# Kernel optimization log

Hardware: AMD Instinct MI355X
Metric: run time of the kernel (lower is better)

## Reference

```python
import jax, jax.numpy as jnp
import numpy as np

B = 4
NB = 8192   # points per batch
MB = 2048   # query points per batch
C_IN = 64
RADII = (0.2, 0.4)
NSAMPLES = (16, 32)
EPS = 1e-5


def setup_inputs() -> dict:
    key = jax.random.key(0)
    ks = jax.random.split(key, 8)
    inp = {}
    inp["xyz"] = jax.random.uniform(ks[0], (B * NB, 3), jnp.float32)
    inp["features"] = jax.random.normal(ks[1], (B * NB, C_IN), jnp.float32)
    inp["new_xyz"] = jax.random.uniform(ks[2], (B * MB, 3), jnp.float32)
    inp["xyz_batch_cnt"] = jnp.full((B,), NB, jnp.int32)
    inp["new_xyz_batch_cnt"] = jnp.full((B,), MB, jnp.int32)
    cin = C_IN + 3  # use_xyz=True concatenates relative xyz
    for s in range(2):
        k0, k1 = jax.random.split(ks[3 + s])
        inp[f"w{s}0"] = jax.random.normal(k0, (128, cin), jnp.float32) * (2.0 / cin) ** 0.5
        inp[f"g{s}0"] = jnp.ones((128,), jnp.float32)
        inp[f"b{s}0"] = jnp.zeros((128,), jnp.float32)
        inp[f"w{s}1"] = jax.random.normal(k1, (128, 128), jnp.float32) * (2.0 / 128) ** 0.5
        inp[f"g{s}1"] = jnp.ones((128,), jnp.float32)
        inp[f"b{s}1"] = jnp.zeros((128,), jnp.float32)
    return inp


def _ball_query(new_b, xyz_b, radius, nsample):
    # new_b: (B, M, 3), xyz_b: (B, N, 3)
    n = xyz_b.shape[1]
    # squared distances via the quadratic expansion (avoids (B,M,N,3) temp)
    d2 = (jnp.sum(new_b * new_b, -1)[:, :, None]
          + jnp.sum(xyz_b * xyz_b, -1)[:, None, :]
          - 2.0 * jnp.einsum('bmc,bnc->bmn', new_b, xyz_b))
    in_ball = d2 < radius * radius
    # first-nsample-in-original-order semantics of the CUDA ball query
    order_key = jnp.where(in_ball, jnp.arange(n, dtype=jnp.int32)[None, None, :], n)
    idxs = jnp.sort(order_key, axis=-1)[..., :nsample]        # (B, M, nsample)
    valid = idxs < n
    first = idxs[..., :1]                                     # pad with first found idx
    idx = jnp.where(valid, idxs, first)
    empty = ~valid[..., 0]                                    # no neighbor in ball
    idx = jnp.where(empty[..., None], 0, idx)
    return idx, empty


def _bn_relu(x, g, b):
    # training-mode BatchNorm2d over (M, nsample) per channel, then ReLU
    mean = jnp.mean(x, axis=(0, 1))
    var = jnp.var(x, axis=(0, 1))
    return jax.nn.relu((x - mean) * jax.lax.rsqrt(var + EPS) * g + b)


def _scale(xyz_b, feat_b, new_b, radius, nsample, w0, g0, b0, w1, g1, b1):
    idx, empty = _ball_query(new_b, xyz_b, radius, nsample)
    gather = jax.vmap(lambda pts, i: pts[i])                  # per-batch gather
    gx = gather(xyz_b, idx) - new_b[:, :, None, :]            # (B, M, ns, 3)
    gf = gather(feat_b, idx)                                  # (B, M, ns, C)
    g = jnp.concatenate([gx, gf], axis=-1)                    # use_xyz=True
    g = jnp.where(empty[..., None, None], 0.0, g)             # zero empty balls
    g = g.reshape(-1, nsample, g.shape[-1])                   # (M_total, ns, 3+C)
    h = _bn_relu(jnp.einsum('mnc,oc->mno', g, w0), g0, b0)    # shared 1x1 conv
    h = _bn_relu(jnp.einsum('mnc,oc->mno', h, w1), g1, b1)
    return jnp.max(h, axis=1)                                 # max_pool over ns


def reference(xyz, features, new_xyz, xyz_batch_cnt, new_xyz_batch_cnt,
              w00, g00, b00, w01, g01, b01,
              w10, g10, b10, w11, g11, b11):
    b = xyz_batch_cnt.shape[0]
    xyz_b = xyz.reshape(b, -1, 3)
    feat_b = features.reshape(b, -1, features.shape[-1])
    new_b = new_xyz.reshape(b, -1, 3)
    f0 = _scale(xyz_b, feat_b, new_b, RADII[0], NSAMPLES[0], w00, g00, b00, w01, g01, b01)
    f1 = _scale(xyz_b, feat_b, new_b, RADII[1], NSAMPLES[1], w10, g10, b10, w11, g11, b11)
    return new_xyz, jnp.concatenate([f0, f1], axis=1)         # (M_total, 256)
```

## Files before the change

kernel.cpp:

```cpp
#include <hip/hip_runtime.h>
#include <stdio.h>

#define NBP   8192
#define MTOT  8192
#define CIN   64
#define CO    128

#define EPR(...) do { fprintf(stderr, __VA_ARGS__); fflush(stderr); } while (0)

typedef short short8 __attribute__((ext_vector_type(8)));
typedef float floatx4 __attribute__((ext_vector_type(4)));
typedef unsigned short ushort;
typedef ushort ushort4v __attribute__((ext_vector_type(4)));

__device__ __forceinline__ ushort f2b(float f)
{
    union { unsigned int i; float f; } x; x.f = f;
    return (ushort)((x.i + 0x7fffu + ((x.i >> 16) & 1u)) >> 16);
}
__device__ __forceinline__ float b2f(ushort u)
{
    union { unsigned int i; float f; } x; x.i = ((unsigned int)u) << 16;
    return x.f;
}
__device__ __forceinline__ void split_rne(float v, ushort& h, ushort& l)
{
    ushort hh = f2b(v);
    h = hh; l = f2b(v - b2f(hh));
}

__global__ void __launch_bounds__(256, 1) StackSAModuleMSG_85761906966880_kernel(
    const float* __restrict__ nxyz, float* __restrict__ out, float* __restrict__ stats,
    const float* __restrict__ feat, ushort* __restrict__ fh,
    const float* __restrict__ xyz, float4* __restrict__ xyz4, double* __restrict__ ppd,
    const float* __restrict__ w00, const float* __restrict__ w01,
    const float* __restrict__ w10, const float* __restrict__ w11,
    ushort* __restrict__ wh00, ushort* __restrict__ wl00,
    ushort* __restrict__ wh01, ushort* __restrict__ wl01,
    ushort* __restrict__ wh10, ushort* __restrict__ wl10,
    ushort* __restrict__ wh11, ushort* __restrict__ wl11)
{
    int i = blockIdx.x * 256 + threadIdx.x;
    if (i < 1024) stats[i] = 0.f;
    if (i < MTOT*3) out[i] = nxyz[i];
    if (i < 128*128) {
        split_rne(w01[i], wh01[i], wl01[i]);
        split_rne(w11[i], wh11[i], wl11[i]);
    }
    if (i < 128*96) {
        int o = i / 96, kd = i - o*96;
        int c = (kd < 64) ? (kd + 3) : ((kd < 67) ? (kd - 64) : -1);
        float a = (c >= 0) ? w00[o*67 + c] : 0.f;
        split_rne(a, wh00[i], wl00[i]);
        float b = (c >= 0) ? w10[o*67 + c] : 0.f;
        split_rne(b, wh10[i], wl10[i]);
    }
    if (i < 4*NBP) {
        float x = xyz[3*i+0], y = xyz[3*i+1], z = xyz[3*i+2];
        xyz4[i] = make_float4(x, y, z, 0.f);
        double px = (double)x, py = (double)y, pz = (double)z;
        ppd[i] = px*px + py*py + pz*pz;
    }
    {
        float4 v = *(const float4*)(feat + (size_t)4*i);
        ushort4v h;
        h[0] = f2b(v.x); h[1] = f2b(v.y); h[2] = f2b(v.z); h[3] = f2b(v.w);
        *(ushort4v*)(fh + (size_t)4*i) = h;
    }
}

__global__ void __launch_bounds__(256, 1) sa_ballq(
    const float4* __restrict__ xyz4, const double* __restrict__ ppd,
    const float* __restrict__ new_xyz,
    int* __restrict__ idx0, int* __restrict__ idx1,
    int* __restrict__ empty0, int* __restrict__ empty1)
{
    const double r2a = 0.2 * 0.2;
    const double r2b = 0.4 * 0.4;
    int m    = blockIdx.x * 4 + (threadIdx.x >> 6);
    int lane = threadIdx.x & 63;
    int b    = m >> 11;
    int base = b * NBP;

    double nx = (double)new_xyz[3*m+0];
    double ny = (double)new_xyz[3*m+1];
    double nz = (double)new_xyz[3*m+2];
    double nn = nx*nx + ny*ny + nz*nz;

    int cnt0 = 0, cnt1 = 0;
    int first0 = base, first1 = base;
    unsigned long long lt = (1ull << lane) - 1ull;

    for (int j = 0; j < NBP; j += 64) {
        int gi = base + j + lane;
        float4 p = xyz4[gi];
        double px = (double)p.x;
        double py = (double)p.y;
        double pz = (double)p.z;
        double pp = ppd[gi];
        double dt = nx*px + ny*py + nz*pz;
        double d2 = nn + pp - 2.0*dt;
        bool in0 = d2 < r2a;
        bool in1 = d2 < r2b;
        unsigned long long m0 = __ballot(in0);
        unsigned long long m1 = __ballot(in1);
        if (in0) {
            int p0 = cnt0 + __popcll(m0 & lt);
            if (p0 < 16) idx0[m*16 + p0] = gi;
        }
        if (in1) {
            int p1 = cnt1 + __popcll(m1 & lt);
            if (p1 < 32) idx1[m*32 + p1] = gi;
        }
        if (cnt0 == 0 && m0) first0 = base + j + (__ffsll((long long)m0) - 1);
        if (cnt1 == 0 && m1) first1 = base + j + (__ffsll((long long)m1) - 1);
        cnt0 += __popcll(m0);
        cnt1 += __popcll(m1);
        if (cnt0 >= 16 && cnt1 >= 32) break;
    }
    int c0 = cnt0 < 16 ? cnt0 : 16;
    int c1 = cnt1 < 32 ? cnt1 : 32;
    if (lane >= c0 && lane < 16) idx0[m*16 + lane] = first0;
    if (lane >= c1 && lane < 32) idx1[m*32 + lane] = first1;
    if (lane == 0) { empty0[m] = (cnt0 == 0); empty1[m] = (cnt1 == 0); }
}

template<int NS, int GM>
__device__ __forceinline__ void stats1_body(
    const ushort* __restrict__ fh,
    const float* __restrict__ xyz, const float* __restrict__ nxyz,
    const int* __restrict__ idx, const int* __restrict__ empty,
    const ushort* __restrict__ wh0, float* __restrict__ part,
    int bx, int t, ushort* ah)
{
    int m0 = bx * GM;
    int wv = t >> 6, lane = t & 63, l16 = lane & 15, qo = lane >> 4;
    int n0 = 32*wv;

    short8 bh[3][2];
#pragma unroll
    for (int ks = 0; ks < 3; ks++)
#pragma unroll
        for (int nt = 0; nt < 2; nt++)
            bh[ks][nt] = *(const short8*)(wh0 +
                (long long)(n0 + 16*nt + l16)*96 + ks*32 + qo*8);

    unsigned em = 0;
#pragma unroll
    for (int g = 0; g < GM; g++) em |= (empty[m0 + g] ? 1u : 0u) << g;
    const long long ib = (long long)m0 * NS;
    int n1 = t >> 3, c8 = t & 7, n2 = n1 + 32;
    int n3 = t >> 2, k3 = t & 3;
    int gi1 = idx[ib + n1];
    int gi2 = idx[ib + n2];
    short8 vh1 = *(const short8*)(fh + (size_t)gi1*CIN + 8*c8);
    short8 vh2 = *(const short8*)(fh + (size_t)gi2*CIN + 8*c8);
    const short8 Z8 = {0,0,0,0,0,0,0,0};
    short8 vh3 = Z8;
    int g3 = n3 / NS;
    if (k3 == 0 && !((em >> g3) & 1u)) {
        int gi3 = idx[ib + n3];
#pragma unroll
        for (int c = 0; c < 3; c++)
            vh3[c] = (short)f2b(xyz[3*gi3+c] - nxyz[3*(m0+g3)+c]);
    }

    if ((em >> (n1 / NS)) & 1u) vh1 = Z8;
    if ((em >> (n2 / NS)) & 1u) vh2 = Z8;
    *(short8*)(ah + n1*136 + 8*c8) = vh1;
    *(short8*)(ah + n2*136 + 8*c8) = vh2;
    *(short8*)(ah + n3*136 + 64 + 8*k3) = vh3;
    __syncthreads();

    floatx4 acc[4][2];
#pragma unroll
    for (int i = 0; i < 4; i++) {
        acc[i][0] = (floatx4){0.f,0.f,0.f,0.f};
        acc[i][1] = (floatx4){0.f,0.f,0.f,0.f};
    }
#pragma unroll
    for (int ks = 0; ks < 3; ks++) {
        int kb = ks*32 + qo*8;
#pragma unroll
        for (int mt = 0; mt < 4; mt++) {
            int ao = (16*mt + l16)*136 + kb;
            short8 fh8 = *(const short8*)(ah + ao);
#pragma unroll
            for (int nt = 0; nt < 2; nt++)
                acc[mt][nt] = __builtin_amdgcn_mfma_f32_16x16x32_bf16(
                                  fh8, bh[ks][nt], acc[mt][nt], 0, 0, 0);
        }
    }

    float sum[2] = {0.f,0.f}, sq[2] = {0.f,0.f};
#pragma unroll
    for (int mt = 0; mt < 4; mt++)
#pragma unroll
        for (int nt = 0; nt < 2; nt++)
#pragma unroll
            for (int r = 0; r < 4; r++) {
                float a = acc[mt][nt][r];
                sum[nt] += a; sq[nt] = fmaf(a, a, sq[nt]);
            }
#pragma unroll
    for (int nt = 0; nt < 2; nt++) {
        sum[nt] += __shfl_xor(sum[nt], 16); sum[nt] += __shfl_xor(sum[nt], 32);
        sq[nt]  += __shfl_xor(sq[nt],  16); sq[nt]  += __shfl_xor(sq[nt],  32);
    }
    if (lane < 16) {
#pragma unroll
        for (int nt = 0; nt < 2; nt++) {
            int c = n0 + 16*nt + lane;
            part[(long long)bx*256 + c]       = sum[nt];
            part[(long long)bx*256 + 128 + c] = sq[nt];
        }
    }
}

__global__ void __launch_bounds__(256, 4) sa_stats1_both(
    const ushort* __restrict__ fh,
    const float* __restrict__ xyz, const float* __restrict__ nxyz,
    const int* __restrict__ idx0, const int* __restrict__ empty0,
    const ushort* __restrict__ wh00, float* __restrict__ partA,
    const int* __restrict__ idx1, const int* __restrict__ empty1,
    const ushort* __restrict__ wh10, float* __restrict__ partB)
{
    __shared__ ushort ah[64*136];
    int t = threadIdx.x;
    if (blockIdx.x < MTOT/4)
        stats1_body<16,4>(fh, xyz, nxyz, idx0, empty0, wh00, partA,
                          blockIdx.x, t, ah);
    else
        stats1_body<32,2>(fh, xyz, nxyz, idx1, empty1, wh10, partB,
                          blockIdx.x - MTOT/4, t, ah);
}

template<int NS, int GM>
__device__ __forceinline__ void fused_body(
    const ushort* __restrict__ fh,
    const float* __restrict__ xyz, const float* __restrict__ nxyz,
    const int* __restrict__ idx, const int* __restrict__ empty,
    const ushort* __restrict__ wh0, const ushort* __restrict__ wl0,
    const ushort* __restrict__ wh1, const ushort* __restrict__ wl1,
    const float* __restrict__ g0, const float* __restrict__ b0,
    const float* __restrict__ s1sum, const float* __restrict__ s1sq,
    float* __restrict__ part, float* __restrict__ mxo, float* __restrict__ mno,
    float invN, int bx, int t,
    ushort* ah, float* kv, float* sv)
{
    const int TPG = NS/16;
    int m0 = bx * GM;
    int wv = t >> 6, lane = t & 63, l16 = lane & 15, qo = lane >> 4;
    int n0 = 32*wv;

    if (t < 128) {
        float mean = s1sum[t] * invN;
        float var  = s1sq[t] * invN - mean * mean;
        float k    = rsqrtf(var + 1e-5f) * g0[t];
        kv[t] = k;
        sv[t] = b0[t] - mean * k;
    }

    short8 b1h[3][2], b1l[3][2];
#pragma unroll
    for (int ks = 0; ks < 3; ks++)
#pragma unroll
        for (int nt = 0; nt < 2; nt++) {
            long long wo = (long long)(n0 + 16*nt + l16)*96 + ks*32 + qo*8;
            b1h[ks][nt] = *(const short8*)(wh0 + wo);
            b1l[ks][nt] = *(const short8*)(wl0 + wo);
        }

    unsigned em = 0;
#pragma unroll
    for (int g = 0; g < GM; g++) em |= (empty[m0 + g] ? 1u : 0u) << g;
    const long long ib = (long long)m0 * NS;
    int n1 = t >> 3, c8 = t & 7, n2 = n1 + 32;
    int n3 = t >> 2, k3 = t & 3;
    int gi1 = idx[ib + n1];
    int gi2 = idx[ib + n2];
    short8 vh1 = *(const short8*)(fh + (size_t)gi1*CIN + 8*c8);
    short8 vh2 = *(const short8*)(fh + (size_t)gi2*CIN + 8*c8);
    const short8 Z8 = {0,0,0,0,0,0,0,0};
    short8 vh3 = Z8;
    int g3 = n3 / NS;
    if (k3 == 0 && !((em >> g3) & 1u)) {
        int gi3 = idx[ib + n3];
#pragma unroll
        for (int c = 0; c < 3; c++)
            vh3[c] = (short)f2b(xyz[3*gi3+c] - nxyz[3*(m0+g3)+c]);
    }

    if ((em >> (n1 / NS)) & 1u) vh1 = Z8;
    if ((em >> (n2 / NS)) & 1u) vh2 = Z8;
    *(short8*)(ah + n1*136 + 8*c8) = vh1;
    *(short8*)(ah + n2*136 + 8*c8) = vh2;
    *(short8*)(ah + n3*136 + 64 + 8*k3) = vh3;
    __syncthreads();

    {
        floatx4 acc[4][2];
#pragma unroll
        for (int i = 0; i < 4; i++) {
            acc[i][0] = (floatx4){0.f,0.f,0.f,0.f};
            acc[i][1] = (floatx4){0.f,0.f,0.f,0.f};
        }
#pragma unroll
        for (int ks = 0; ks < 3; ks++) {
            int kb = ks*32 + qo*8;
#pragma unroll
            for (int mt = 0; mt < 4; mt++) {
                int ao = (16*mt + l16)*136 + kb;
                short8 fh8 = *(const short8*)(ah + ao);
#pragma unroll
                for (int nt = 0; nt < 2; nt++) {
                    acc[mt][nt] = __builtin_amdgcn_mfma_f32_16x16x32_bf16(
                                      fh8, b1l[ks][nt], acc[mt][nt], 0, 0, 0);
                    acc[mt][nt] = __builtin_amdgcn_mfma_f32_16x16x32_bf16(
                                      fh8, b1h[ks][nt], acc[mt][nt], 0, 0, 0);
                }
            }
        }

        __syncthreads();
#pragma unroll
        for (int nt = 0; nt < 2; nt++) {
            int c = n0 + 16*nt + l16;
            float k = kv[c], s = sv[c];
#pragma unroll
            for (int mt = 0; mt < 4; mt++) {
#pragma unroll
                for (int r = 0; r < 4; r++) {
                    float h = fmaxf(fmaf(acc[mt][nt][r], k, s), 0.f);
                    int row = 16*mt + qo*4 + r;
                    ah[row*136 + c] = f2b(h);
                }
            }
        }

        short8 b2h[4][2], b2l[4][2];
#pragma unroll
        for (int ks = 0; ks < 4; ks++)
#pragma unroll
            for (int nt = 0; nt < 2; nt++) {
                long long wo = (long long)(n0 + 16*nt + l16)*128 + ks*32 + qo*8;
                b2h[ks][nt] = *(const short8*)(wh1 + wo);
                b2l[ks][nt] = *(const short8*)(wl1 + wo);
            }
        __syncthreads();

        floatx4 acc2[4][2];
#pragma unroll
        for (int i = 0; i < 4; i++) {
            acc2[i][0] = (floatx4){0.f,0.f,0.f,0.f};
            acc2[i][1] = (floatx4){0.f,0.f,0.f,0.f};
        }
#pragma unroll
        for (int ks = 0; ks < 4; ks++) {
            int kb = ks*32 + qo*8;
#pragma unroll
            for (int mt = 0; mt < 4; mt++) {
                int ao = (16*mt + l16)*136 + kb;
                short8 fh8 = *(const short8*)(ah + ao);
#pragma unroll
                for (int nt = 0; nt < 2; nt++) {
                    acc2[mt][nt] = __builtin_amdgcn_mfma_f32_16x16x32_bf16(
                                      fh8, b2l[ks][nt], acc2[mt][nt], 0, 0, 0);
                    acc2[mt][nt] = __builtin_amdgcn_mfma_f32_16x16x32_bf16(
                                      fh8, b2h[ks][nt], acc2[mt][nt], 0, 0, 0);
                }
            }
        }

        float sum[2] = {0.f,0.f}, sq[2] = {0.f,0.f};
        float Mx[GM][2], Mn[GM][2];
#pragma unroll
        for (int g = 0; g < GM; g++) {
            Mx[g][0] = -3.4e38f; Mx[g][1] = -3.4e38f;
            Mn[g][0] =  3.4e38f; Mn[g][1] =  3.4e38f;
        }
#pragma unroll
        for (int mt = 0; mt < 4; mt++) {
            int gg = mt / TPG;
#pragma unroll
            for (int nt = 0; nt < 2; nt++)
#pragma unroll
                for (int r = 0; r < 4; r++) {
                    float a = acc2[mt][nt][r];
                    sum[nt] += a; sq[nt] = fmaf(a, a, sq[nt]);
                    Mx[gg][nt] = fmaxf(Mx[gg][nt], a);
                    Mn[gg][nt] = fminf(Mn[gg][nt], a);
                }
        }
#pragma unroll
        for (int nt = 0; nt < 2; nt++) {
            sum[nt] += __shfl_xor(sum[nt], 16); sum[nt] += __shfl_xor(sum[nt], 32);
            sq[nt]  += __shfl_xor(sq[nt],  16); sq[nt]  += __shfl_xor(sq[nt],  32);
#pragma unroll
            for (int g = 0; g < GM; g++) {
                Mx[g][nt] = fmaxf(Mx[g][nt], __shfl_xor(Mx[g][nt], 16));
                Mx[g][nt] = fmaxf(Mx[g][nt], __shfl_xor(Mx[g][nt], 32));
                Mn[g][nt] = fminf(Mn[g][nt], __shfl_xor(Mn[g][nt], 16));
                Mn[g][nt] = fminf(Mn[g][nt], __shfl_xor(Mn[g][nt], 32));
            }
        }
        if (lane < 16) {
#pragma unroll
            for (int nt = 0; nt < 2; nt++) {
                int c = n0 + 16*nt + lane;
                part[(long long)bx*256 + c]       = sum[nt];
                part[(long long)bx*256 + 128 + c] = sq[nt];
#pragma unroll
                for (int g = 0; g < GM; g++) {
                    mxo[(long long)(m0+g)*128 + c] = Mx[g][nt];
                    mno[(long long)(m0+g)*128 + c] = Mn[g][nt];
                }
            }
        }
    }
}

__global__ void __launch_bounds__(256, 4) sa_fused_both(
    const ushort* __restrict__ fh,
    const float* __restrict__ xyz, const float* __restrict__ nxyz,
    const int* __restrict__ idx0, const int* __restrict__ empty0,
    const ushort* __restrict__ wh00, const ushort* __restrict__ wl00,
    const ushort* __restrict__ wh01, const ushort* __restrict__ wl01,
    const float* __restrict__ g00, const float* __restrict__ b00,
    const float* __restrict__ s1sumA, const float* __restrict__ s1sqA,
    float* __restrict__ partA, float* __restrict__ mx0, float* __restrict__ mn0,
    float invN0,
    const int* __restrict__ idx1, const int* __restrict__ empty1,
    const ushort* __restrict__ wh10, const ushort* __restrict__ wl10,
    const ushort* __restrict__ wh11, const ushort* __restrict__ wl11,
    const float* __restrict__ g10, const float* __restrict__ b10,
    const float* __restrict__ s1sumB, const float* __restrict__ s1sqB,
    float* __restrict__ partB, float* __restrict__ mx1, float* __restrict__ mn1,
    float invN1)
{
    __shared__ ushort ah[64*136];
    __shared__ float kv[128], sv[128];
    int t = threadIdx.x;
    if (blockIdx.x < MTOT/4)
        fused_body<16,4>(fh, xyz, nxyz, idx0, empty0,
                         wh00, wl00, wh01, wl01, g00, b00, s1sumA, s1sqA,
                         partA, mx0, mn0, invN0, blockIdx.x, t,
                         ah, kv, sv);
    else
        fused_body<32,2>(fh, xyz, nxyz, idx1, empty1,
                         wh10, wl10, wh11, wl11, g10, b10, s1sumB, s1sqB,
                         partB, mx1, mn1, invN1, blockIdx.x - MTOT/4, t,
                         ah, kv, sv);
}

__global__ void __launch_bounds__(256, 1) sa_reduce2(
    const float* __restrict__ partA, int nbA, float* __restrict__ dstA,
    const float* __restrict__ partB, int nbB, float* __restrict__ dstB)
{
    __shared__ float red[256];
    int t = threadIdx.x;
    const float* part; float* dst; int nb, b;
    if (blockIdx.x < 256) { part = partA; dst = dstA; nb = nbA; b = blockIdx.x; }
    else                  { part = partB; dst = dstB; nb = nbB; b = blockIdx.x - 256; }
    float s = 0.f;
    for (int i = t; i < nb; i += 256) s += part[(long long)i*256 + b];
    red[t] = s;
    __syncthreads();
    for (int off = 128; off > 0; off >>= 1) {
        if (t < off) red[t] += red[t + off];
        __syncthreads();
    }
    if (t == 0) dst[b] = red[0];
}

__global__ void __launch_bounds__(256, 1) sa_pass3b(
    const float* __restrict__ mx0, const float* __restrict__ mn0,
    const float* __restrict__ g01, const float* __restrict__ b01,
    const float* __restrict__ mx1, const float* __restrict__ mn1,
    const float* __restrict__ g11, const float* __restrict__ b11,
    const float* __restrict__ stats, float* __restrict__ outp,
    float invN0, float invN1)
{
    int i = blockIdx.x * 256 + threadIdx.x;
    int m = i >> 8, o = i & 255;
    bool sc1 = o >= 128;
    int oc = o & 127;
    const float* sm = sc1 ? (stats + 768) : (stats + 256);
    const float* sp = sc1 ? (stats + 896) : (stats + 384);
    float invN = sc1 ? invN1 : invN0;
    float gg   = sc1 ? g11[oc] : g01[oc];
    float bb   = sc1 ? b11[oc] : b01[oc];
    float mean = sm[oc] * invN;
    float var  = sp[oc] * invN - mean * mean;
    float k    = rsqrtf(var + 1e-5f) * gg;
    float sh   = bb - mean * k;
    long long mi = (long long)m * 128 + oc;
    float v;
    if (k >= 0.f) v = sc1 ? mx1[mi] : mx0[mi];
    else          v = sc1 ? mn1[mi] : mn0[mi];
    float r = fmaf(v, k, sh);
    outp[i] = r > 0.f ? r : 0.f;
}

extern "C" void kernel_launch(void* const* d_in, const int* in_sizes, int n_in,
                              void* d_out, int out_size, void* d_ws, size_t ws_size,
                              hipStream_t stream)
{
    const float* xyz  = (const float*)d_in[0];
    const float* feat = (const float*)d_in[1];
    const float* nxyz = (const float*)d_in[2];
    const float* w00 = (const float*)d_in[5];
    const float* g00 = (const float*)d_in[6];
    const float* b00 = (const float*)d_in[7];
    const float* w01 = (const float*)d_in[8];
    const float* g01 = (const float*)d_in[9];
    const float* b01 = (const float*)d_in[10];
    const float* w10 = (const float*)d_in[11];
    const float* g10 = (const float*)d_in[12];
    const float* b10 = (const float*)d_in[13];
    const float* w11 = (const float*)d_in[14];
    const float* g11 = (const float*)d_in[15];
    const float* b11 = (const float*)d_in[16];
    float* out = (float*)d_out;

    char*  wsb    = (char*)d_ws;
    float* stats  = (float*)(wsb);
    int*   idx0   = (int*)(wsb + 4096);
    int*   idx1   = (int*)(wsb + 4096 + 524288);
    int*   empty0 = (int*)(wsb + 4096 + 524288 + 1048576);
    int*   empty1 = (int*)(wsb + 4096 + 524288 + 1048576 + 32768);
    ushort* fh    = (ushort*)(wsb + 2000000);
    float4* xyz4  = (float4*)(wsb + 13000000);
    double* ppd   = (double*)(wsb + 14000000);
    float* mx0    = (float*)(wsb + 150000000);
    float* mn0    = (float*)(wsb + 155000000);
    float* mx1    = (float*)(wsb + 160000000);
    float* mn1    = (float*)(wsb + 165000000);
    ushort* wh01  = (ushort*)(wsb + 170000000);
    ushort* wl01  = (ushort*)(wsb + 171000000);
    ushort* wh11  = (ushort*)(wsb + 172000000);
    ushort* wl11  = (ushort*)(wsb + 173000000);
    ushort* wh00  = (ushort*)(wsb + 174000000);
    ushort* wl00  = (ushort*)(wsb + 175000000);
    ushort* wh10  = (ushort*)(wsb + 176000000);
    ushort* wl10  = (ushort*)(wsb + 177000000);
    float* partA  = (float*)(wsb + 180000000);
    float* partB  = (float*)(wsb + 183000000);

    const float invN0 = 1.0f / (float)(MTOT*16);
    const float invN1 = 1.0f / (float)(MTOT*32);
    float* fout = out + MTOT*3;

    StackSAModuleMSG_85761906966880_kernel<<<2048, 256, 0, stream>>>(
        nxyz, out, stats, feat, fh, xyz, xyz4, ppd,
        w00, w01, w10, w11,
        wh00, wl00, wh01, wl01, wh10, wl10, wh11, wl11);

    sa_ballq<<<MTOT/4, 256, 0, stream>>>(xyz4, ppd, nxyz, idx0, idx1, empty0, empty1);

    sa_stats1_both<<<MTOT/4 + MTOT/2, 256, 0, stream>>>(
        fh, xyz, nxyz,
        idx0, empty0, wh00, partA,
        idx1, empty1, wh10, partB);

    sa_reduce2<<<512, 256, 0, stream>>>(partA, MTOT/4, stats + 0,
                                        partB, MTOT/2, stats + 512);

    sa_fused_both<<<MTOT/4 + MTOT/2, 256, 0, stream>>>(
        fh, xyz, nxyz,
        idx0, empty0, wh00, wl00, wh01, wl01, g00, b00,
        stats + 0, stats + 128, partA, mx0, mn0, invN0,
        idx1, empty1, wh10, wl10, wh11, wl11, g10, b10,
        stats + 512, stats + 640, partB, mx1, mn1, invN1);

    sa_reduce2<<<512, 256, 0, stream>>>(partA, MTOT/4, stats + 256,
                                        partB, MTOT/2, stats + 768);

    sa_pass3b<<<(MTOT*256)/256, 256, 0, stream>>>(
        mx0, mn0, g01, b01, mx1, mn1, g11, b11, stats, fout, invN0, invN1);

    hipError_t e = hipGetLastError();
    if (e != hipSuccess) EPR("[KL] enqueue err=%d (%s)\n", (int)e, hipGetErrorString(e));
}
```

Baseline: 239.7 us.

## Fuse ball query into prep kernel and replace partial-sum reductions with atomics

The ball-query kernel is merged into the preprocessing kernel as extra blocks. It now reads raw xyz and computes squared norms inline, so the float4/double staging buffers are no longer needed. The per-block partial BN statistics and the two separate reduce kernels are replaced by atomicAdd into the stats array, removing three launches and their global round trips. The A tile's LDS stride shrinks and a separate LDS buffer holds the hidden activations, which removes one __syncthreads. Weight register loads are also moved later, after the gathers. The cost is float atomic contention on 512 addresses and a summation order that is no longer deterministic.

```diff
diff --git a/kernel.cpp b/kernel.cpp
--- a/kernel.cpp
+++ b/kernel.cpp
@@ -5,6 +5,8 @@
 #define MTOT  8192
 #define CIN   64
 #define CO    128
+#define ASTR  104
+#define HSTR  136
 
 #define EPR(...) do { fprintf(stderr, __VA_ARGS__); fflush(stderr); } while (0)
 
@@ -30,9 +32,11 @@
 }
 
 __global__ void __launch_bounds__(256, 1) StackSAModuleMSG_85761906966880_kernel(
-    const float* __restrict__ nxyz, float* __restrict__ out, float* __restrict__ stats,
+    const float* __restrict__ xyz, const float* __restrict__ nxyz,
+    float* __restrict__ out, float* __restrict__ stats,
     const float* __restrict__ feat, ushort* __restrict__ fh,
-    const float* __restrict__ xyz, float4* __restrict__ xyz4, double* __restrict__ ppd,
+    int* __restrict__ idx0, int* __restrict__ idx1,
+    int* __restrict__ empty0, int* __restrict__ empty1,
     const float* __restrict__ w00, const float* __restrict__ w01,
     const float* __restrict__ w10, const float* __restrict__ w11,
     ushort* __restrict__ wh00, ushort* __restrict__ wl00,
@@ -40,89 +44,77 @@
     ushort* __restrict__ wh10, ushort* __restrict__ wl10,
     ushort* __restrict__ wh11, ushort* __restrict__ wl11)
 {
-    int i = blockIdx.x * 256 + threadIdx.x;
-    if (i < 1024) stats[i] = 0.f;
-    if (i < MTOT*3) out[i] = nxyz[i];
-    if (i < 128*128) {
-        split_rne(w01[i], wh01[i], wl01[i]);
-        split_rne(w11[i], wh11[i], wl11[i]);
-    }
-    if (i < 128*96) {
-        int o = i / 96, kd = i - o*96;
-        int c = (kd < 64) ? (kd + 3) : ((kd < 67) ? (kd - 64) : -1);
-        float a = (c >= 0) ? w00[o*67 + c] : 0.f;
-        split_rne(a, wh00[i], wl00[i]);
-        float b = (c >= 0) ? w10[o*67 + c] : 0.f;
-        split_rne(b, wh10[i], wl10[i]);
-    }
-    if (i < 4*NBP) {
-        float x = xyz[3*i+0], y = xyz[3*i+1], z = xyz[3*i+2];
-        xyz4[i] = make_float4(x, y, z, 0.f);
-        double px = (double)x, py = (double)y, pz = (double)z;
-        ppd[i] = px*px + py*py + pz*pz;
-    }
-    {
-        float4 v = *(const float4*)(feat + (size_t)4*i);
-        ushort4v h;
-        h[0] = f2b(v.x); h[1] = f2b(v.y); h[2] = f2b(v.z); h[3] = f2b(v.w);
-        *(ushort4v*)(fh + (size_t)4*i) = h;
-    }
-}
-
-__global__ void __launch_bounds__(256, 1) sa_ballq(
-    const float4* __restrict__ xyz4, const double* __restrict__ ppd,
-    const float* __restrict__ new_xyz,
-    int* __restrict__ idx0, int* __restrict__ idx1,
-    int* __restrict__ empty0, int* __restrict__ empty1)
-{
-    const double r2a = 0.2 * 0.2;
-    const double r2b = 0.4 * 0.4;
-    int m    = blockIdx.x * 4 + (threadIdx.x >> 6);
-    int lane = threadIdx.x & 63;
-    int b    = m >> 11;
-    int base = b * NBP;
-
-    double nx = (double)new_xyz[3*m+0];
-    double ny = (double)new_xyz[3*m+1];
-    double nz = (double)new_xyz[3*m+2];
-    double nn = nx*nx + ny*ny + nz*nz;
-
-    int cnt0 = 0, cnt1 = 0;
-    int first0 = base, first1 = base;
-    unsigned long long lt = (1ull << lane) - 1ull;
-
-    for (int j = 0; j < NBP; j += 64) {
-        int gi = base + j + lane;
-        float4 p = xyz4[gi];
-        double px = (double)p.x;
-        double py = (double)p.y;
-        double pz = (double)p.z;
-        double pp = ppd[gi];
-        double dt = nx*px + ny*py + nz*pz;
-        double d2 = nn + pp - 2.0*dt;
-        bool in0 = d2 < r2a;
-        bool in1 = d2 < r2b;
-        unsigned long long m0 = __ballot(in0);
-        unsigned long long m1 = __ballot(in1);
-        if (in0) {
-            int p0 = cnt0 + __popcll(m0 & lt);
-            if (p0 < 16) idx0[m*16 + p0] = gi;
-        }
-        if (in1) {
-            int p1 = cnt1 + __popcll(m1 & lt);
-            if (p1 < 32) idx1[m*32 + p1] = gi;
-        }
-        if (cnt0 == 0 && m0) first0 = base + j + (__ffsll((long long)m0) - 1);
-        if (cnt1 == 0 && m1) first1 = base + j + (__ffsll((long long)m1) - 1);
-        cnt0 += __popcll(m0);
-        cnt1 += __popcll(m1);
-        if (cnt0 >= 16 && cnt1 >= 32) break;
-    }
-    int c0 = cnt0 < 16 ? cnt0 : 16;
-    int c1 = cnt1 < 32 ? cnt1 : 32;
-    if (lane >= c0 && lane < 16) idx0[m*16 + lane] = first0;
-    if (lane >= c1 && lane < 32) idx1[m*32 + lane] = first1;
-    if (lane == 0) { empty0[m] = (cnt0 == 0); empty1[m] = (cnt1 == 0); }
+    if (blockIdx.x < MTOT/4) {
+        const double r2a = 0.2 * 0.2;
+        const double r2b = 0.4 * 0.4;
+        int m    = blockIdx.x * 4 + (threadIdx.x >> 6);
+        int lane = threadIdx.x & 63;
+        int b    = m >> 11;
+        int base = b * NBP;
+
+        double nx = (double)nxyz[3*m+0];
+        double ny = (double)nxyz[3*m+1];
+        double nz = (double)nxyz[3*m+2];
+        double nn = nx*nx + ny*ny + nz*nz;
+
+        int cnt0 = 0, cnt1 = 0;
+        int first0 = base, first1 = base;
+        unsigned long long lt = (1ull << lane) - 1ull;
+
+        for (int j = 0; j < NBP; j += 64) {
+            int gi = base + j + lane;
+            double px = (double)xyz[3*gi+0];
+            double py = (double)xyz[3*gi+1];
+            double pz = (double)xyz[3*gi+2];
+            double pp = px*px + py*py + pz*pz;
+            double dt = nx*px + ny*py + nz*pz;
+            double d2 = nn + pp - 2.0*dt;
+            bool in0 = d2 < r2a;
+            bool in1 = d2 < r2b;
+            unsigned long long m0 = __ballot(in0);
+            unsigned long long m1 = __ballot(in1);
+            if (in0) {
+                int p0 = cnt0 + __popcll(m0 & lt);
+                if (p0 < 16) idx0[m*16 + p0] = gi;
+            }
+            if (in1) {
+                int p1 = cnt1 + __popcll(m1 & lt);
+                if (p1 < 32) idx1[m*32 + p1] = gi;
+            }
+            if (cnt0 == 0 && m0) first0 = base + j + (__ffsll((long long)m0) - 1);
+            if (cnt1 == 0 && m1) first1 = base + j + (__ffsll((long long)m1) - 1);
+            cnt0 += __popcll(m0);
+            cnt1 += __popcll(m1);
+            if (cnt0 >= 16 && cnt1 >= 32) break;
+        }
+        int c0 = cnt0 < 16 ? cnt0 : 16;
+        int c1 = cnt1 < 32 ? cnt1 : 32;
+        if (lane >= c0 && lane < 16) idx0[m*16 + lane] = first0;
+        if (lane >= c1 && lane < 32) idx1[m*32 + lane] = first1;
+        if (lane == 0) { empty0[m] = (cnt0 == 0); empty1[m] = (cnt1 == 0); }
+    } else {
+        int i = (blockIdx.x - MTOT/4) * 256 + threadIdx.x;
+        if (i < 1024) stats[i] = 0.f;
+        if (i < MTOT*3) out[i] = nxyz[i];
+        if (i < 128*128) {
+            split_rne(w01[i], wh01[i], wl01[i]);
+            split_rne(w11[i], wh11[i], wl11[i]);
+        }
+        if (i < 128*96) {
+            int o = i / 96, kd = i - o*96;
+            int c = (kd < 64) ? (kd + 3) : ((kd < 67) ? (kd - 64) : -1);
+            float a = (c >= 0) ? w00[o*67 + c] : 0.f;
+            split_rne(a, wh00[i], wl00[i]);
+            float b = (c >= 0) ? w10[o*67 + c] : 0.f;
+            split_rne(b, wh10[i], wl10[i]);
+        }
+        {
+            float4 v = *(const float4*)(feat + (size_t)4*i);
+            ushort4v h;
+            h[0] = f2b(v.x); h[1] = f2b(v.y); h[2] = f2b(v.z); h[3] = f2b(v.w);
+            *(ushort4v*)(fh + (size_t)4*i) = h;
+        }
+    }
 }
 
 template<int NS, int GM>
@@ -130,20 +122,13 @@
     const ushort* __restrict__ fh,
     const float* __restrict__ xyz, const float* __restrict__ nxyz,
     const int* __restrict__ idx, const int* __restrict__ empty,
-    const ushort* __restrict__ wh0, float* __restrict__ part,
+    const ushort* __restrict__ wh0,
+    float* __restrict__ ssum, float* __restrict__ ssq,
     int bx, int t, ushort* ah)
 {
     int m0 = bx * GM;
     int wv = t >> 6, lane = t & 63, l16 = lane & 15, qo = lane >> 4;
     int n0 = 32*wv;
-
-    short8 bh[3][2];
-#pragma unroll
-    for (int ks = 0; ks < 3; ks++)
-#pragma unroll
-        for (int nt = 0; nt < 2; nt++)
-            bh[ks][nt] = *(const short8*)(wh0 +
-                (long long)(n0 + 16*nt + l16)*96 + ks*32 + qo*8);
 
     unsigned em = 0;
 #pragma unroll
@@ -165,11 +150,19 @@
             vh3[c] = (short)f2b(xyz[3*gi3+c] - nxyz[3*(m0+g3)+c]);
     }
 
+    short8 bh[3][2];
+#pragma unroll
+    for (int ks = 0; ks < 3; ks++)
+#pragma unroll
+        for (int nt = 0; nt < 2; nt++)
+            bh[ks][nt] = *(const short8*)(wh0 +
+                (long long)(n0 + 16*nt + l16)*96 + ks*32 + qo*8);
+
     if ((em >> (n1 / NS)) & 1u) vh1 = Z8;
     if ((em >> (n2 / NS)) & 1u) vh2 = Z8;
-    *(short8*)(ah + n1*136 + 8*c8) = vh1;
-    *(short8*)(ah + n2*136 + 8*c8) = vh2;
-    *(short8*)(ah + n3*136 + 64 + 8*k3) = vh3;
+    *(short8*)(ah + n1*ASTR + 8*c8) = vh1;
+    *(short8*)(ah + n2*ASTR + 8*c8) = vh2;
+    *(short8*)(ah + n3*ASTR + 64 + 8*k3) = vh3;
     __syncthreads();
 
     floatx4 acc[4][2];
@@ -183,7 +176,7 @@
         int kb = ks*32 + qo*8;
 #pragma unroll
         for (int mt = 0; mt < 4; mt++) {
-            int ao = (16*mt + l16)*136 + kb;
+            int ao = (16*mt + l16)*ASTR + kb;
             short8 fh8 = *(const short8*)(ah + ao);
 #pragma unroll
             for (int nt = 0; nt < 2; nt++)
@@ -211,8 +204,8 @@
 #pragma unroll
         for (int nt = 0; nt < 2; nt++) {
             int c = n0 + 16*nt + lane;
-            part[(long long)bx*256 + c]       = sum[nt];
-            part[(long long)bx*256 + 128 + c] = sq[nt];
+            atomicAdd(&ssum[c], sum[nt]);
+            atomicAdd(&ssq[c],  sq[nt]);
         }
     }
 }
@@ -221,18 +214,18 @@
     const ushort* __restrict__ fh,
     const float* __restrict__ xyz, const float* __restrict__ nxyz,
     const int* __restrict__ idx0, const int* __restrict__ empty0,
-    const ushort* __restrict__ wh00, float* __restrict__ partA,
+    const ushort* __restrict__ wh00, float* __restrict__ stats,
     const int* __restrict__ idx1, const int* __restrict__ empty1,
-    const ushort* __restrict__ wh10, float* __restrict__ partB)
-{
-    __shared__ ushort ah[64*136];
+    const ushort* __restrict__ wh10)
+{
+    __shared__ ushort ah[64*ASTR];
     int t = threadIdx.x;
     if (blockIdx.x < MTOT/4)
-        stats1_body<16,4>(fh, xyz, nxyz, idx0, empty0, wh00, partA,
-                          blockIdx.x, t, ah);
+        stats1_body<16,4>(fh, xyz, nxyz, idx0, empty0, wh00,
+                          stats + 0, stats + 128, blockIdx.x, t, ah);
     else
-        stats1_body<32,2>(fh, xyz, nxyz, idx1, empty1, wh10, partB,
-                          blockIdx.x - MTOT/4, t, ah);
+        stats1_body<32,2>(fh, xyz, nxyz, idx1, empty1, wh10,
+                          stats + 512, stats + 640, blockIdx.x - MTOT/4, t, ah);
 }
 
 template<int NS, int GM>
@@ -244,9 +237,10 @@
     const ushort* __restrict__ wh1, const ushort* __restrict__ wl1,
     const float* __restrict__ g0, const float* __restrict__ b0,
     const float* __restrict__ s1sum, const float* __restrict__ s1sq,
-    float* __restrict__ part, float* __restrict__ mxo, float* __restrict__ mno,
+    float* __restrict__ s2sum, float* __restrict__ s2sq,
+    float* __restrict__ mxo, float* __restrict__ mno,
     float invN, int bx, int t,
-    ushort* ah, float* kv, float* sv)
+    ushort* ah, ushort* bh, float* kv, float* sv)
 {
     const int TPG = NS/16;
     int m0 = bx * GM;
@@ -260,16 +254,6 @@
         kv[t] = k;
         sv[t] = b0[t] - mean * k;
     }
-
-    short8 b1h[3][2], b1l[3][2];
-#pragma unroll
-    for (int ks = 0; ks < 3; ks++)
-#pragma unroll
-        for (int nt = 0; nt < 2; nt++) {
-            long long wo = (long long)(n0 + 16*nt + l16)*96 + ks*32 + qo*8;
-            b1h[ks][nt] = *(const short8*)(wh0 + wo);
-            b1l[ks][nt] = *(const short8*)(wl0 + wo);
-        }
 
     unsigned em = 0;
 #pragma unroll
@@ -291,11 +275,21 @@
             vh3[c] = (short)f2b(xyz[3*gi3+c] - nxyz[3*(m0+g3)+c]);
     }
 
+    short8 b1h[3][2], b1l[3][2];
+#pragma unroll
+    for (int ks = 0; ks < 3; ks++)
+#pragma unroll
+        for (int nt = 0; nt < 2; nt++) {
+            long long wo = (long long)(n0 + 16*nt + l16)*96 + ks*32 + qo*8;
+            b1h[ks][nt] = *(const short8*)(wh0 + wo);
+            b1l[ks][nt] = *(const short8*)(wl0 + wo);
+        }
+
     if ((em >> (n1 / NS)) & 1u) vh1 = Z8;
     if ((em >> (n2 / NS)) & 1u) vh2 = Z8;
-    *(short8*)(ah + n1*136 + 8*c8) = vh1;
-    *(short8*)(ah + n2*136 + 8*c8) = vh2;
-    *(short8*)(ah + n3*136 + 64 + 8*k3) = vh3;
+    *(short8*)(ah + n1*ASTR + 8*c8) = vh1;
+    *(short8*)(ah + n2*ASTR + 8*c8) = vh2;
+    *(short8*)(ah + n3*ASTR + 64 + 8*k3) = vh3;
     __syncthreads();
 
     {
@@ -310,7 +304,7 @@
             int kb = ks*32 + qo*8;
 #pragma unroll
             for (int mt = 0; mt < 4; mt++) {
-                int ao = (16*mt + l16)*136 + kb;
+                int ao = (16*mt + l16)*ASTR + kb;
                 short8 fh8 = *(const short8*)(ah + ao);
 #pragma unroll
                 for (int nt = 0; nt < 2; nt++) {
@@ -322,22 +316,6 @@
             }
         }
 
-        __syncthreads();
-#pragma unroll
-        for (int nt = 0; nt < 2; nt++) {
-            int c = n0 + 16*nt + l16;
-            float k = kv[c], s = sv[c];
-#pragma unroll
-            for (int mt = 0; mt < 4; mt++) {
-#pragma unroll
-                for (int r = 0; r < 4; r++) {
-                    float h = fmaxf(fmaf(acc[mt][nt][r], k, s), 0.f);
-                    int row = 16*mt + qo*4 + r;
-                    ah[row*136 + c] = f2b(h);
-                }
-            }
-        }
-
         short8 b2h[4][2], b2l[4][2];
 #pragma unroll
         for (int ks = 0; ks < 4; ks++)
@@ -347,6 +325,21 @@
                 b2h[ks][nt] = *(const short8*)(wh1 + wo);
                 b2l[ks][nt] = *(const short8*)(wl1 + wo);
             }
+
+#pragma unroll
+        for (int nt = 0; nt < 2; nt++) {
+            int c = n0 + 16*nt + l16;
+            float k = kv[c], s = sv[c];
+#pragma unroll
+            for (int mt = 0; mt < 4; mt++) {
+#pragma unroll
+                for (int r = 0; r < 4; r++) {
+                    float h = fmaxf(fmaf(acc[mt][nt][r], k, s), 0.f);
+                    int row = 16*mt + qo*4 + r;
+                    bh[row*HSTR + c] = f2b(h);
+                }
+            }
+        }
         __syncthreads();
 
         floatx4 acc2[4][2];
@@ -360,8 +353,8 @@
             int kb = ks*32 + qo*8;
 #pragma unroll
             for (int mt = 0; mt < 4; mt++) {
-                int ao = (16*mt + l16)*136 + kb;
-                short8 fh8 = *(const short8*)(ah + ao);
+                int ao = (16*mt + l16)*HSTR + kb;
+                short8 fh8 = *(const short8*)(bh + ao);
 #pragma unroll
                 for (int nt = 0; nt < 2; nt++) {
                     acc2[mt][nt] = __builtin_amdgcn_mfma_f32_16x16x32_bf16(
@@ -408,8 +401,8 @@
 #pragma unroll
             for (int nt = 0; nt < 2; nt++) {
                 int c = n0 + 16*nt + lane;
-                part[(long long)bx*256 + c]       = sum[nt];
-                part[(long long)bx*256 + 128 + c] = sq[nt];
+                atomicAdd(&s2sum[c], sum[nt]);
+                atomicAdd(&s2sq[c],  sq[nt]);
 #pragma unroll
                 for (int g = 0; g < GM; g++) {
                     mxo[(long long)(m0+g)*128 + c] = Mx[g][nt];
@@ -427,50 +420,28 @@
     const ushort* __restrict__ wh00, const ushort* __restrict__ wl00,
     const ushort* __restrict__ wh01, const ushort* __restrict__ wl01,
     const float* __restrict__ g00, const float* __restrict__ b00,
-    const float* __restrict__ s1sumA, const float* __restrict__ s1sqA,
-    float* __restrict__ partA, float* __restrict__ mx0, float* __restrict__ mn0,
-    float invN0,
+    float* __restrict__ stats,
+    float* __restrict__ mx0, float* __restrict__ mn0, float invN0,
     const int* __restrict__ idx1, const int* __restrict__ empty1,
     const ushort* __restrict__ wh10, const ushort* __restrict__ wl10,
     const ushort* __restrict__ wh11, const ushort* __restrict__ wl11,
     const float* __restrict__ g10, const float* __restrict__ b10,
-    const float* __restrict__ s1sumB, const float* __restrict__ s1sqB,
-    float* __restrict__ partB, float* __restrict__ mx1, float* __restrict__ mn1,
-    float invN1)
-{
-    __shared__ ushort ah[64*136];
+    float* __restrict__ mx1, float* __restrict__ mn1, float invN1)
+{
+    __shared__ ushort ah[64*ASTR];
+    __shared__ ushort bh[64*HSTR];
     __shared__ float kv[128], sv[128];
     int t = threadIdx.x;
     if (blockIdx.x < MTOT/4)
         fused_body<16,4>(fh, xyz, nxyz, idx0, empty0,
-                         wh00, wl00, wh01, wl01, g00, b00, s1sumA, s1sqA,
-                         partA, mx0, mn0, invN0, blockIdx.x, t,
-                         ah, kv, sv);
+                         wh00, wl00, wh01, wl01, g00, b00,
+                         stats + 0, stats + 128, stats + 256, stats + 384,
+                         mx0, mn0, invN0, blockIdx.x, t, ah, bh, kv, sv);
     else
         fused_body<32,2>(fh, xyz, nxyz, idx1, empty1,
-                         wh10, wl10, wh11, wl11, g10, b10, s1sumB, s1sqB,
-                         partB, mx1, mn1, invN1, blockIdx.x - MTOT/4, t,
-                         ah, kv, sv);
-}
-
-__global__ void __launch_bounds__(256, 1) sa_reduce2(
-    const float* __restrict__ partA, int nbA, float* __restrict__ dstA,
-    const float* __restrict__ partB, int nbB, float* __restrict__ dstB)
-{
-    __shared__ float red[256];
-    int t = threadIdx.x;
-    const float* part; float* dst; int nb, b;
-    if (blockIdx.x < 256) { part = partA; dst = dstA; nb = nbA; b = blockIdx.x; }
-    else                  { part = partB; dst = dstB; nb = nbB; b = blockIdx.x - 256; }
-    float s = 0.f;
-    for (int i = t; i < nb; i += 256) s += part[(long long)i*256 + b];
-    red[t] = s;
-    __syncthreads();
-    for (int off = 128; off > 0; off >>= 1) {
-        if (t < off) red[t] += red[t + off];
-        __syncthreads();
-    }
-    if (t == 0) dst[b] = red[0];
+                         wh10, wl10, wh11, wl11, g10, b10,
+                         stats + 512, stats + 640, stats + 768, stats + 896,
+                         mx1, mn1, invN1, blockIdx.x - MTOT/4, t, ah, bh, kv, sv);
 }
 
 __global__ void __launch_bounds__(256, 1) sa_pass3b(
@@ -530,8 +501,6 @@
     int*   empty0 = (int*)(wsb + 4096 + 524288 + 1048576);
     int*   empty1 = (int*)(wsb + 4096 + 524288 + 1048576 + 32768);
     ushort* fh    = (ushort*)(wsb + 2000000);
-    float4* xyz4  = (float4*)(wsb + 13000000);
-    double* ppd   = (double*)(wsb + 14000000);
     float* mx0    = (float*)(wsb + 150000000);
     float* mn0    = (float*)(wsb + 155000000);
     float* mx1    = (float*)(wsb + 160000000);
@@ -544,37 +513,28 @@
     ushort* wl00  = (ushort*)(wsb + 175000000);
     ushort* wh10  = (ushort*)(wsb + 176000000);
     ushort* wl10  = (ushort*)(wsb + 177000000);
-    float* partA  = (float*)(wsb + 180000000);
-    float* partB  = (float*)(wsb + 183000000);
 
     const float invN0 = 1.0f / (float)(MTOT*16);
     const float invN1 = 1.0f / (float)(MTOT*32);
     float* fout = out + MTOT*3;
 
-    StackSAModuleMSG_85761906966880_kernel<<<2048, 256, 0, stream>>>(
-        nxyz, out, stats, feat, fh, xyz, xyz4, ppd,
+    StackSAModuleMSG_85761906966880_kernel<<<MTOT/4 + 2048, 256, 0, stream>>>(
+        xyz, nxyz, out, stats, feat, fh,
+        idx0, idx1, empty0, empty1,
         w00, w01, w10, w11,
         wh00, wl00, wh01, wl01, wh10, wl10, wh11, wl11);
 
-    sa_ballq<<<MTOT/4, 256, 0, stream>>>(xyz4, ppd, nxyz, idx0, idx1, empty0, empty1);
-
     sa_stats1_both<<<MTOT/4 + MTOT/2, 256, 0, stream>>>(
         fh, xyz, nxyz,
-        idx0, empty0, wh00, partA,
-        idx1, empty1, wh10, partB);
-
-    sa_reduce2<<<512, 256, 0, stream>>>(partA, MTOT/4, stats + 0,
-                                        partB, MTOT/2, stats + 512);
+        idx0, empty0, wh00, stats,
+        idx1, empty1, wh10);
 
     sa_fused_both<<<MTOT/4 + MTOT/2, 256, 0, stream>>>(
         fh, xyz, nxyz,
         idx0, empty0, wh00, wl00, wh01, wl01, g00, b00,
-        stats + 0, stats + 128, partA, mx0, mn0, invN0,
+        stats, mx0, mn0, invN0,
         idx1, empty1, wh10, wl10, wh11, wl11, g10, b10,
-        stats + 512, stats + 640, partB, mx1, mn1, invN1);
-
-    sa_reduce2<<<512, 256, 0, stream>>>(partA, MTOT/4, stats + 256,
-                                        partB, MTOT/2, stats + 768);
+        mx1, mn1, invN1);
 
     sa_pass3b<<<(MTOT*256)/256, 256, 0, stream>>>(
         mx0, mn0, g01, b01, mx1, mn1, g11, b11, stats, fout, invN0, invN1);
```

New measurement: 397.0 us. 1.66x slower.

## Merge ball query into prep kernel and raise occupancy bounds on MLP kernels

Applied to the files above, without the earlier changes.

The ball-query kernel is folded into the preprocessing kernel as extra blocks, so one launch and the xyz4/ppd intermediate buffers go away. Ball query now reads the packed xyz directly and computes |p|^2 in double on the fly. This is safe because the ball query never read fh or the split weights. Separately, launch_bounds min-blocks on the stats1 and fused kernels rises from 4 to 6, which can force register spilling. The unaligned 3-float loads and the per-iteration recompute of |p|^2 add some cost in the ball-query loop.

```diff
diff --git a/kernel.cpp b/kernel.cpp
--- a/kernel.cpp
+++ b/kernel.cpp
@@ -30,9 +30,11 @@
 }
 
 __global__ void __launch_bounds__(256, 1) StackSAModuleMSG_85761906966880_kernel(
-    const float* __restrict__ nxyz, float* __restrict__ out, float* __restrict__ stats,
+    const float* __restrict__ xyz, const float* __restrict__ nxyz,
+    float* __restrict__ out, float* __restrict__ stats,
     const float* __restrict__ feat, ushort* __restrict__ fh,
-    const float* __restrict__ xyz, float4* __restrict__ xyz4, double* __restrict__ ppd,
+    int* __restrict__ idx0, int* __restrict__ idx1,
+    int* __restrict__ empty0, int* __restrict__ empty1,
     const float* __restrict__ w00, const float* __restrict__ w01,
     const float* __restrict__ w10, const float* __restrict__ w11,
     ushort* __restrict__ wh00, ushort* __restrict__ wl00,
@@ -40,89 +42,77 @@
     ushort* __restrict__ wh10, ushort* __restrict__ wl10,
     ushort* __restrict__ wh11, ushort* __restrict__ wl11)
 {
-    int i = blockIdx.x * 256 + threadIdx.x;
-    if (i < 1024) stats[i] = 0.f;
-    if (i < MTOT*3) out[i] = nxyz[i];
-    if (i < 128*128) {
-        split_rne(w01[i], wh01[i], wl01[i]);
-        split_rne(w11[i], wh11[i], wl11[i]);
-    }
-    if (i < 128*96) {
-        int o = i / 96, kd = i - o*96;
-        int c = (kd < 64) ? (kd + 3) : ((kd < 67) ? (kd - 64) : -1);
-        float a = (c >= 0) ? w00[o*67 + c] : 0.f;
-        split_rne(a, wh00[i], wl00[i]);
-        float b = (c >= 0) ? w10[o*67 + c] : 0.f;
-        split_rne(b, wh10[i], wl10[i]);
-    }
-    if (i < 4*NBP) {
-        float x = xyz[3*i+0], y = xyz[3*i+1], z = xyz[3*i+2];
-        xyz4[i] = make_float4(x, y, z, 0.f);
-        double px = (double)x, py = (double)y, pz = (double)z;
-        ppd[i] = px*px + py*py + pz*pz;
-    }
-    {
-        float4 v = *(const float4*)(feat + (size_t)4*i);
-        ushort4v h;
-        h[0] = f2b(v.x); h[1] = f2b(v.y); h[2] = f2b(v.z); h[3] = f2b(v.w);
-        *(ushort4v*)(fh + (size_t)4*i) = h;
-    }
-}
-
-__global__ void __launch_bounds__(256, 1) sa_ballq(
-    const float4* __restrict__ xyz4, const double* __restrict__ ppd,
-    const float* __restrict__ new_xyz,
-    int* __restrict__ idx0, int* __restrict__ idx1,
-    int* __restrict__ empty0, int* __restrict__ empty1)
-{
-    const double r2a = 0.2 * 0.2;
-    const double r2b = 0.4 * 0.4;
-    int m    = blockIdx.x * 4 + (threadIdx.x >> 6);
-    int lane = threadIdx.x & 63;
-    int b    = m >> 11;
-    int base = b * NBP;
-
-    double nx = (double)new_xyz[3*m+0];
-    double ny = (double)new_xyz[3*m+1];
-    double nz = (double)new_xyz[3*m+2];
-    double nn = nx*nx + ny*ny + nz*nz;
-
-    int cnt0 = 0, cnt1 = 0;
-    int first0 = base, first1 = base;
-    unsigned long long lt = (1ull << lane) - 1ull;
-
-    for (int j = 0; j < NBP; j += 64) {
-        int gi = base + j + lane;
-        float4 p = xyz4[gi];
-        double px = (double)p.x;
-        double py = (double)p.y;
-        double pz = (double)p.z;
-        double pp = ppd[gi];
-        double dt = nx*px + ny*py + nz*pz;
-        double d2 = nn + pp - 2.0*dt;
-        bool in0 = d2 < r2a;
-        bool in1 = d2 < r2b;
-        unsigned long long m0 = __ballot(in0);
-        unsigned long long m1 = __ballot(in1);
-        if (in0) {
-            int p0 = cnt0 + __popcll(m0 & lt);
-            if (p0 < 16) idx0[m*16 + p0] = gi;
-        }
-        if (in1) {
-            int p1 = cnt1 + __popcll(m1 & lt);
-            if (p1 < 32) idx1[m*32 + p1] = gi;
-        }
-        if (cnt0 == 0 && m0) first0 = base + j + (__ffsll((long long)m0) - 1);
-        if (cnt1 == 0 && m1) first1 = base + j + (__ffsll((long long)m1) - 1);
-        cnt0 += __popcll(m0);
-        cnt1 += __popcll(m1);
-        if (cnt0 >= 16 && cnt1 >= 32) break;
-    }
-    int c0 = cnt0 < 16 ? cnt0 : 16;
-    int c1 = cnt1 < 32 ? cnt1 : 32;
-    if (lane >= c0 && lane < 16) idx0[m*16 + lane] = first0;
-    if (lane >= c1 && lane < 32) idx1[m*32 + lane] = first1;
-    if (lane == 0) { empty0[m] = (cnt0 == 0); empty1[m] = (cnt1 == 0); }
+    if (blockIdx.x < MTOT/4) {
+        const double r2a = 0.2 * 0.2;
+        const double r2b = 0.4 * 0.4;
+        int m    = blockIdx.x * 4 + (threadIdx.x >> 6);
+        int lane = threadIdx.x & 63;
+        int b    = m >> 11;
+        int base = b * NBP;
+
+        double nx = (double)nxyz[3*m+0];
+        double ny = (double)nxyz[3*m+1];
+        double nz = (double)nxyz[3*m+2];
+        double nn = nx*nx + ny*ny + nz*nz;
+
+        int cnt0 = 0, cnt1 = 0;
+        int first0 = base, first1 = base;
+        unsigned long long lt = (1ull << lane) - 1ull;
+
+        for (int j = 0; j < NBP; j += 64) {
+            int gi = base + j + lane;
+            double px = (double)xyz[3*gi+0];
+            double py = (double)xyz[3*gi+1];
+            double pz = (double)xyz[3*gi+2];
+            double pp = px*px + py*py + pz*pz;
+            double dt = nx*px + ny*py + nz*pz;
+            double d2 = nn + pp - 2.0*dt;
+            bool in0 = d2 < r2a;
+            bool in1 = d2 < r2b;
+            unsigned long long m0 = __ballot(in0);
+            unsigned long long m1 = __ballot(in1);
+            if (in0) {
+                int p0 = cnt0 + __popcll(m0 & lt);
+                if (p0 < 16) idx0[m*16 + p0] = gi;
+            }
+            if (in1) {
+                int p1 = cnt1 + __popcll(m1 & lt);
+                if (p1 < 32) idx1[m*32 + p1] = gi;
+            }
+            if (cnt0 == 0 && m0) first0 = base + j + (__ffsll((long long)m0) - 1);
+            if (cnt1 == 0 && m1) first1 = base + j + (__ffsll((long long)m1) - 1);
+            cnt0 += __popcll(m0);
+            cnt1 += __popcll(m1);
+            if (cnt0 >= 16 && cnt1 >= 32) break;
+        }
+        int c0 = cnt0 < 16 ? cnt0 : 16;
+        int c1 = cnt1 < 32 ? cnt1 : 32;
+        if (lane >= c0 && lane < 16) idx0[m*16 + lane] = first0;
+        if (lane >= c1 && lane < 32) idx1[m*32 + lane] = first1;
+        if (lane == 0) { empty0[m] = (cnt0 == 0); empty1[m] = (cnt1 == 0); }
+    } else {
+        int i = (blockIdx.x - MTOT/4) * 256 + threadIdx.x;
+        if (i < 1024) stats[i] = 0.f;
+        if (i < MTOT*3) out[i] = nxyz[i];
+        if (i < 128*128) {
+            split_rne(w01[i], wh01[i], wl01[i]);
+            split_rne(w11[i], wh11[i], wl11[i]);
+        }
+        if (i < 128*96) {
+            int o = i / 96, kd = i - o*96;
+            int c = (kd < 64) ? (kd + 3) : ((kd < 67) ? (kd - 64) : -1);
+            float a = (c >= 0) ? w00[o*67 + c] : 0.f;
+            split_rne(a, wh00[i], wl00[i]);
+            float b = (c >= 0) ? w10[o*67 + c] : 0.f;
+            split_rne(b, wh10[i], wl10[i]);
+        }
+        {
+            float4 v = *(const float4*)(feat + (size_t)4*i);
+            ushort4v h;
+            h[0] = f2b(v.x); h[1] = f2b(v.y); h[2] = f2b(v.z); h[3] = f2b(v.w);
+            *(ushort4v*)(fh + (size_t)4*i) = h;
+        }
+    }
 }
 
 template<int NS, int GM>
@@ -217,7 +207,7 @@
     }
 }
 
-__global__ void __launch_bounds__(256, 4) sa_stats1_both(
+__global__ void __launch_bounds__(256, 6) sa_stats1_both(
     const ushort* __restrict__ fh,
     const float* __restrict__ xyz, const float* __restrict__ nxyz,
     const int* __restrict__ idx0, const int* __restrict__ empty0,
@@ -420,7 +410,7 @@
     }
 }
 
-__global__ void __launch_bounds__(256, 4) sa_fused_both(
+__global__ void __launch_bounds__(256, 6) sa_fused_both(
     const ushort* __restrict__ fh,
     const float* __restrict__ xyz, const float* __restrict__ nxyz,
     const int* __restrict__ idx0, const int* __restrict__ empty0,
@@ -530,8 +520,6 @@
     int*   empty0 = (int*)(wsb + 4096 + 524288 + 1048576);
     int*   empty1 = (int*)(wsb + 4096 + 524288 + 1048576 + 32768);
     ushort* fh    = (ushort*)(wsb + 2000000);
-    float4* xyz4  = (float4*)(wsb + 13000000);
-    double* ppd   = (double*)(wsb + 14000000);
     float* mx0    = (float*)(wsb + 150000000);
     float* mn0    = (float*)(wsb + 155000000);
     float* mx1    = (float*)(wsb + 160000000);
@@ -551,12 +539,11 @@
     const float invN1 = 1.0f / (float)(MTOT*32);
     float* fout = out + MTOT*3;
 
-    StackSAModuleMSG_85761906966880_kernel<<<2048, 256, 0, stream>>>(
-        nxyz, out, stats, feat, fh, xyz, xyz4, ppd,
+    StackSAModuleMSG_85761906966880_kernel<<<MTOT/4 + 2048, 256, 0, stream>>>(
+        xyz, nxyz, out, stats, feat, fh,
+        idx0, idx1, empty0, empty1,
         w00, w01, w10, w11,
         wh00, wl00, wh01, wl01, wh10, wl10, wh11, wl11);
-
-    sa_ballq<<<MTOT/4, 256, 0, stream>>>(xyz4, ppd, nxyz, idx0, idx1, empty0, empty1);
 
     sa_stats1_both<<<MTOT/4 + MTOT/2, 256, 0, stream>>>(
         fh, xyz, nxyz,
```

New measurement: 256.7 us. 7.1% more time.
